# Kernel optimization log

Measured on AMD Instinct MI355X. Metric: run time of the kernel, lower is better.

The kernel has to match this reference:

```python
import jax, jax.numpy as jnp
import numpy as np

NEG_POS_RATIO = 3
THETA = 0.01
NUM_CLASSES = 21
B, P = 64, 16320
POS_FRAC = 0.02


def setup_inputs() -> dict:
    key = jax.random.key(0)
    k1, k2, k3, k4, k5, k6 = jax.random.split(key, 6)
    loc_data = jax.random.normal(k1, (B, P, 4), dtype=jnp.float32)
    conf_data = jax.random.normal(k2, (B, P, NUM_CLASSES), dtype=jnp.float32)
    arm_conf_data = jax.random.normal(k3, (B, P, 2), dtype=jnp.float32)
    loc_t = jax.random.normal(k4, (B, P, 4), dtype=jnp.float32)
    labels = jax.random.randint(k5, (B, P), 1, NUM_CLASSES)
    is_pos = jax.random.uniform(k6, (B, P)) < POS_FRAC
    conf_t = jnp.where(is_pos, labels, 0).astype(jnp.int64)
    return {"loc_data": loc_data, "conf_data": conf_data,
            "arm_conf_data": arm_conf_data, "loc_t": loc_t, "conf_t": conf_t}


def _multibox_loss(loc_data, conf_data, arm_conf_data, loc_t, conf_t):
    num_priors = conf_t.shape[1]
    # ODM: zero out positives whose ARM objectness score P(obj) <= theta
    p_obj = jax.nn.softmax(arm_conf_data, axis=-1)[:, :, 1]          # [B,P]
    pos = (conf_t > 0) & (p_obj > THETA)                             # [B,P]

    # localization loss: smooth L1 over positive anchors (masked sum == masked gather + sum)
    diff = loc_data - loc_t
    ad = jnp.abs(diff)
    sl1 = jnp.where(ad < 1.0, 0.5 * ad * ad, ad - 0.5)               # [B,P,4]
    loss_l = jnp.sum(sl1 * pos[..., None].astype(sl1.dtype))

    # per-anchor CE loss: logsumexp(c) - c[target]
    lse = jax.nn.logsumexp(conf_data, axis=-1)                       # [B,P]
    true_logit = jnp.take_along_axis(conf_data, conf_t[..., None], axis=-1)[..., 0]
    loss_c_all = lse - true_logit                                    # [B,P]

    # hard negative mining: rank non-positive anchors by loss (double argsort)
    loss_for_rank = jnp.where(pos, 0.0, loss_c_all)
    rank = jnp.argsort(jnp.argsort(-loss_for_rank, axis=1), axis=1)  # [B,P]
    num_pos = jnp.sum(pos.astype(jnp.int32), axis=1, keepdims=True)  # [B,1]
    num_neg = jnp.minimum(NEG_POS_RATIO * num_pos, num_priors - 1)
    neg = rank < num_neg                                             # [B,P]

    sel = pos | neg
    loss_c = jnp.sum(jnp.where(sel, loss_c_all, 0.0))

    N = jnp.sum(num_pos).astype(loss_l.dtype)
    return loss_l / N, loss_c / N


def reference(loc_data, conf_data, arm_conf_data, loc_t, conf_t):
    return _multibox_loss(loc_data, conf_data, arm_conf_data, loc_t, conf_t)
```

## Files before the change

kernel.cpp:

```cpp
#include <hip/hip_runtime.h>

#define NUM_P 16320
#define NUM_C 21
#define THETA 0.01f
#define WAVES_PER_ROW (NUM_P / 64)

__global__ __launch_bounds__(256) void anchor_kernel(
    const float* __restrict__ loc, const float* __restrict__ conf,
    const float* __restrict__ arm, const float* __restrict__ loct,
    const int* __restrict__ conft,
    int* __restrict__ partial_n, float* __restrict__ rankvals,
    float* __restrict__ partial_l, float* __restrict__ partial_c, int total)
{
    __shared__ float tile[256 * NUM_C];
    __shared__ float red_l[4], red_c[4];
    const int tid = threadIdx.x;
    const int base = blockIdx.x * 256;
    const int a = base + tid;

    int t = 0; float2 av = make_float2(0.f, 0.f);
    if (a < total) {
        t = conft[a];
        av = ((const float2*)arm)[a];
    }

    {
        const float4* conf4 = (const float4*)(conf + (size_t)base * NUM_C);
        const int lim = min(256 * NUM_C / 4, ((total - base) * NUM_C) / 4);
        float4 r[6];
        #pragma unroll
        for (int it = 0; it < 6; ++it) {
            int i = tid + it * 256;
            if (i < lim) r[it] = conf4[i];
        }
        float4* tile4 = (float4*)tile;
        #pragma unroll
        for (int it = 0; it < 6; ++it) {
            int i = tid + it * 256;
            if (i < lim) tile4[i] = r[it];
        }
    }
    __syncthreads();

    float ll = 0.f, cep = 0.f;
    bool pos = false;
    if (a < total) {
        const float* cf = &tile[tid * NUM_C];
        float mx = cf[0];
        #pragma unroll
        for (int j = 1; j < NUM_C; ++j) mx = fmaxf(mx, cf[j]);
        float s = 0.f;
        #pragma unroll
        for (int j = 0; j < NUM_C; ++j) s += __expf(cf[j] - mx);
        const float ce = mx + __logf(s) - cf[t];

        const float am = fmaxf(av.x, av.y);
        const float e0 = __expf(av.x - am), e1 = __expf(av.y - am);
        const float p1 = e1 / (e0 + e1);
        pos = (t > 0) && (p1 > THETA);

        if (pos) {
            cep = ce;
            const float4 lv = ((const float4*)loc)[a];
            const float4 tv = ((const float4*)loct)[a];
            const float dx[4] = { lv.x - tv.x, lv.y - tv.y, lv.z - tv.z, lv.w - tv.w };
            #pragma unroll
            for (int j = 0; j < 4; ++j) {
                float ad = fabsf(dx[j]);
                ll += (ad < 1.f) ? 0.5f * ad * ad : ad - 0.5f;
            }
        }
        rankvals[a] = pos ? 0.f : ce;
    }

    unsigned long long pm = __ballot(pos);
    #pragma unroll
    for (int off = 32; off > 0; off >>= 1) {
        ll  += __shfl_down(ll, off, 64);
        cep += __shfl_down(cep, off, 64);
    }
    const int lane = tid & 63, w = tid >> 6;
    if (lane == 0) {
        red_l[w] = ll;
        red_c[w] = cep;
        if (base + (w << 6) < total)
            partial_n[blockIdx.x * 4 + w] = (int)__popcll(pm);
    }
    __syncthreads();
    if (tid == 0) {
        partial_l[blockIdx.x] = red_l[0] + red_l[1] + red_l[2] + red_l[3];
        partial_c[blockIdx.x] = red_c[0] + red_c[1] + red_c[2] + red_c[3];
    }
}

__global__ __launch_bounds__(1024) void select_kernel(
    const float* __restrict__ rankvals, const int* __restrict__ partial_n,
    float* __restrict__ topk, int* __restrict__ row_npos)
{
    __shared__ float data[NUM_P];
    __shared__ int hist[256];
    __shared__ unsigned s_prefix;
    __shared__ int s_kk;
    __shared__ int s_np;
    __shared__ float wsum[16];

    const int b = blockIdx.x;
    const int tid = threadIdx.x;
    const int lane = tid & 63;

    const float4* row4 = (const float4*)(rankvals + (size_t)b * NUM_P);
    float4 r[4];
    #pragma unroll
    for (int it = 0; it < 4; ++it) {
        int i = tid + it * 1024;
        if (i < NUM_P / 4) r[it] = row4[i];
    }
    int rn = (tid < WAVES_PER_ROW) ? partial_n[b * WAVES_PER_ROW + tid] : 0;
    if (tid == 0) s_np = 0;
    if (tid < 256) hist[tid] = 0;
    {
        float4* d4 = (float4*)data;
        #pragma unroll
        for (int it = 0; it < 4; ++it) {
            int i = tid + it * 1024;
            if (i < NUM_P / 4) d4[i] = r[it];
        }
    }
    __syncthreads();

    #pragma unroll
    for (int off = 32; off > 0; off >>= 1) rn += __shfl_down(rn, off, 64);
    if (lane == 0 && rn) atomicAdd(&s_np, rn);
    __syncthreads();

    const int np = s_np;
    const int k = min(3 * np, NUM_P - 1);
    if (k <= 0) {
        if (tid == 0) { topk[b] = 0.f; row_npos[b] = np; }
        return;
    }

    unsigned prefix = 0, himask = 0;
    int kk = k;

    for (int pass = 0; pass < 4; ++pass) {
        const int shift = 24 - 8 * pass;

        if (pass == 0) {
            for (int it = 0; it < 16; ++it) {
                const int i = tid + it * 1024;
                const bool part = i < NUM_P;
                const unsigned u = part ? __float_as_uint(data[i]) : 0u;
                const unsigned bin = u >> 24;
                unsigned long long alive = __ballot(part);
                while (alive) {
                    const int leader = __ffsll(alive) - 1;
                    const unsigned lb = __shfl(bin, leader, 64);
                    const unsigned long long mm = __ballot(part && (bin == lb));
                    if (lane == leader) atomicAdd(&hist[lb], (int)__popcll(mm));
                    alive &= ~mm;
                }
            }
        } else {
            for (int it = 0; it < 16; ++it) {
                const int i = tid + it * 1024;
                if (i < NUM_P) {
                    const unsigned u = __float_as_uint(data[i]);
                    if ((u & himask) == prefix)
                        atomicAdd(&hist[(u >> shift) & 255u], 1);
                }
            }
        }
        __syncthreads();

        if (tid < 64) {
            const int j0 = tid * 4;
            const int h0 = hist[j0], h1 = hist[j0 + 1], h2 = hist[j0 + 2], h3 = hist[j0 + 3];
            int ssum = h0 + h1 + h2 + h3;
            #pragma unroll
            for (int d = 1; d < 64; d <<= 1) {
                const int tmp = __shfl_down(ssum, d, 64);
                if (lane + d < 64) ssum += tmp;
            }
            const int bse = ssum - (h0 + h1 + h2 + h3);
            int S[5];
            S[0] = ssum;
            S[3] = bse + h3;
            S[2] = S[3] + h2;
            S[1] = S[2] + h1;
            S[4] = bse;
            #pragma unroll
            for (int jj = 0; jj < 4; ++jj) {
                if (S[jj] >= kk && S[jj + 1] < kk) {
                    s_prefix = prefix | ((unsigned)(j0 + jj) << shift);
                    s_kk = kk - S[jj + 1];
                }
            }
        }
        __syncthreads();
        prefix = s_prefix;
        kk = s_kk;
        himask |= (0xFFu << shift);
        if (tid < 256) hist[tid] = 0;
        __syncthreads();
    }

    const unsigned vbits = prefix;
    const float vth = __uint_as_float(vbits);

    float partial = 0.f;
    for (int it = 0; it < 16; ++it) {
        const int i = tid + it * 1024;
        if (i < NUM_P) {
            const float x = data[i];
            if (__float_as_uint(x) > vbits) partial += x;
        }
    }
    #pragma unroll
    for (int off = 32; off > 0; off >>= 1)
        partial += __shfl_down(partial, off, 64);
    if (lane == 0) wsum[tid >> 6] = partial;
    __syncthreads();
    if (tid == 0) {
        float tot = 0.f;
        #pragma unroll
        for (int wv = 0; wv < 16; ++wv) tot += wsum[wv];
        topk[b] = tot + (float)kk * vth;
        row_npos[b] = np;
    }
}

__global__ __launch_bounds__(256) void finalize_kernel(
    const float* __restrict__ topk, const int* __restrict__ row_npos,
    const float* __restrict__ partial_l, const float* __restrict__ partial_c,
    int nblocks, int Bn, float* __restrict__ out)
{
    __shared__ float sl[4], sc[4];
    __shared__ int sn[4];
    const int tid = threadIdx.x;
    float l = 0.f, c = 0.f;
    for (int i = tid; i < nblocks; i += 256) { l += partial_l[i]; c += partial_c[i]; }
    int np = 0;
    for (int i = tid; i < Bn; i += 256) np += row_npos[i];
    for (int i = tid; i < Bn; i += 256) c += topk[i];
    #pragma unroll
    for (int off = 32; off > 0; off >>= 1) {
        l  += __shfl_down(l, off, 64);
        c  += __shfl_down(c, off, 64);
        np += __shfl_down(np, off, 64);
    }
    if ((tid & 63) == 0) { sl[tid >> 6] = l; sc[tid >> 6] = c; sn[tid >> 6] = np; }
    __syncthreads();
    if (tid == 0) {
        const float L = sl[0] + sl[1] + sl[2] + sl[3];
        const float C = sc[0] + sc[1] + sc[2] + sc[3];
        const float N = (float)(sn[0] + sn[1] + sn[2] + sn[3]);
        out[0] = L / N;
        out[1] = C / N;
    }
}

extern "C" void kernel_launch(void* const* d_in, const int* in_sizes, int n_in,
                              void* d_out, int out_size, void* d_ws, size_t ws_size,
                              hipStream_t stream) {
    const float* loc  = (const float*)d_in[0];
    const float* conf = (const float*)d_in[1];
    const float* arm  = (const float*)d_in[2];
    const float* loct = (const float*)d_in[3];
    const int*  conft = (const int*)d_in[4];
    float* out = (float*)d_out;

    const int total = in_sizes[4];
    const int Bn = total / NUM_P;
    const int grid = (total + 255) / 256;

    float* topk      = (float*)d_ws;
    int*   row_npos  = (int*)((char*)d_ws + 256);
    float* partial_l = (float*)((char*)d_ws + 1024);
    float* partial_c = (float*)((char*)d_ws + 17408);
    int*   partial_n = (int*)((char*)d_ws + 33792);
    float* rankvals  = (float*)((char*)d_ws + 99328);

    hipLaunchKernelGGL(anchor_kernel, dim3(grid), dim3(256), 0, stream,
                       loc, conf, arm, loct, conft, partial_n, rankvals,
                       partial_l, partial_c, total);
    hipLaunchKernelGGL(select_kernel, dim3(Bn), dim3(1024), 0, stream,
                       rankvals, partial_n, topk, row_npos);
    hipLaunchKernelGGL(finalize_kernel, dim3(1), dim3(256), 0, stream,
                       topk, row_npos, partial_l, partial_c, grid, Bn, out);
}
```

Before: 214.9 us.

## Persistent prefetching anchor kernel, register-resident select, fuse finalize via atomics

The anchor kernel becomes a persistent grid-stride loop that prefetches the next tile's conf, conf_t and arm data into registers while computing the current tile. The select kernel keeps each row in registers instead of copying it to shared memory, and also reduces a slice of the loc/conf partials. The separate finalize kernel is removed: blocks accumulate into global atomics and the last-arriving block writes the output, which requires a memset of the accumulator before launch. Float atomics make the summation order nondeterministic, and the tail guards are dropped, so the code assumes the total is a multiple of 256.

```diff
diff --git a/kernel.cpp b/kernel.cpp
--- a/kernel.cpp
+++ b/kernel.cpp
@@ -10,253 +10,279 @@
     const float* __restrict__ arm, const float* __restrict__ loct,
     const int* __restrict__ conft,
     int* __restrict__ partial_n, float* __restrict__ rankvals,
-    float* __restrict__ partial_l, float* __restrict__ partial_c, int total)
+    float* __restrict__ partial_l, float* __restrict__ partial_c,
+    int ntiles)
 {
     __shared__ float tile[256 * NUM_C];
     __shared__ float red_l[4], red_c[4];
     const int tid = threadIdx.x;
-    const int base = blockIdx.x * 256;
-    const int a = base + tid;
-
-    int t = 0; float2 av = make_float2(0.f, 0.f);
-    if (a < total) {
-        t = conft[a];
-        av = ((const float2*)arm)[a];
-    }
+    const int lane = tid & 63, w = tid >> 6;
+    const int stride = gridDim.x;
+
+    int t = blockIdx.x;
+    if (t >= ntiles) return;
+
+    float4 rr[6];
+    int    tc_n;
+    float2 av_n;
 
     {
+        const int base = t * 256;
         const float4* conf4 = (const float4*)(conf + (size_t)base * NUM_C);
-        const int lim = min(256 * NUM_C / 4, ((total - base) * NUM_C) / 4);
-        float4 r[6];
         #pragma unroll
         for (int it = 0; it < 6; ++it) {
-            int i = tid + it * 256;
-            if (i < lim) r[it] = conf4[i];
-        }
-        float4* tile4 = (float4*)tile;
-        #pragma unroll
-        for (int it = 0; it < 6; ++it) {
-            int i = tid + it * 256;
-            if (i < lim) tile4[i] = r[it];
-        }
-    }
-    __syncthreads();
-
-    float ll = 0.f, cep = 0.f;
-    bool pos = false;
-    if (a < total) {
-        const float* cf = &tile[tid * NUM_C];
-        float mx = cf[0];
-        #pragma unroll
-        for (int j = 1; j < NUM_C; ++j) mx = fmaxf(mx, cf[j]);
-        float s = 0.f;
-        #pragma unroll
-        for (int j = 0; j < NUM_C; ++j) s += __expf(cf[j] - mx);
-        const float ce = mx + __logf(s) - cf[t];
-
-        const float am = fmaxf(av.x, av.y);
-        const float e0 = __expf(av.x - am), e1 = __expf(av.y - am);
-        const float p1 = e1 / (e0 + e1);
-        pos = (t > 0) && (p1 > THETA);
-
-        if (pos) {
-            cep = ce;
-            const float4 lv = ((const float4*)loc)[a];
-            const float4 tv = ((const float4*)loct)[a];
-            const float dx[4] = { lv.x - tv.x, lv.y - tv.y, lv.z - tv.z, lv.w - tv.w };
-            #pragma unroll
-            for (int j = 0; j < 4; ++j) {
-                float ad = fabsf(dx[j]);
-                ll += (ad < 1.f) ? 0.5f * ad * ad : ad - 0.5f;
-            }
-        }
-        rankvals[a] = pos ? 0.f : ce;
-    }
-
-    unsigned long long pm = __ballot(pos);
-    #pragma unroll
-    for (int off = 32; off > 0; off >>= 1) {
-        ll  += __shfl_down(ll, off, 64);
-        cep += __shfl_down(cep, off, 64);
-    }
-    const int lane = tid & 63, w = tid >> 6;
-    if (lane == 0) {
-        red_l[w] = ll;
-        red_c[w] = cep;
-        if (base + (w << 6) < total)
-            partial_n[blockIdx.x * 4 + w] = (int)__popcll(pm);
-    }
-    __syncthreads();
-    if (tid == 0) {
-        partial_l[blockIdx.x] = red_l[0] + red_l[1] + red_l[2] + red_l[3];
-        partial_c[blockIdx.x] = red_c[0] + red_c[1] + red_c[2] + red_c[3];
+            const int i = tid + it * 256;
+            if (i < 1344) rr[it] = conf4[i];
+        }
+        tc_n = conft[base + tid];
+        av_n = ((const float2*)arm)[base + tid];
+    }
+
+    while (true) {
+        const int a = t * 256 + tid;
+        const int    tc = tc_n;
+        const float2 av = av_n;
+
+        {
+            float4* tile4 = (float4*)tile;
+            #pragma unroll
+            for (int it = 0; it < 6; ++it) {
+                const int i = tid + it * 256;
+                if (i < 1344) tile4[i] = rr[it];
+            }
+        }
+        __syncthreads();
+
+        const int tn = t + stride;
+        if (tn < ntiles) {
+            const int nbase = tn * 256;
+            const float4* conf4 = (const float4*)(conf + (size_t)nbase * NUM_C);
+            #pragma unroll
+            for (int it = 0; it < 6; ++it) {
+                const int i = tid + it * 256;
+                if (i < 1344) rr[it] = conf4[i];
+            }
+            tc_n = conft[nbase + tid];
+            av_n = ((const float2*)arm)[nbase + tid];
+        }
+
+        float ll = 0.f, cep = 0.f;
+        bool pos = false;
+        {
+            const float* cf = &tile[tid * NUM_C];
+            float mx = cf[0];
+            #pragma unroll
+            for (int j = 1; j < NUM_C; ++j) mx = fmaxf(mx, cf[j]);
+            float s = 0.f;
+            #pragma unroll
+            for (int j = 0; j < NUM_C; ++j) s += __expf(cf[j] - mx);
+            const float ce = mx + __logf(s) - cf[tc];
+
+            const float am = fmaxf(av.x, av.y);
+            const float e0 = __expf(av.x - am), e1 = __expf(av.y - am);
+            const float p1 = e1 / (e0 + e1);
+            pos = (tc > 0) && (p1 > THETA);
+
+            if (pos) {
+                cep = ce;
+                const float4 lv = ((const float4*)loc)[a];
+                const float4 tv = ((const float4*)loct)[a];
+                const float dx[4] = { lv.x - tv.x, lv.y - tv.y, lv.z - tv.z, lv.w - tv.w };
+                #pragma unroll
+                for (int j = 0; j < 4; ++j) {
+                    const float ad = fabsf(dx[j]);
+                    ll += (ad < 1.f) ? 0.5f * ad * ad : ad - 0.5f;
+                }
+            }
+            rankvals[a] = pos ? 0.f : ce;
+        }
+
+        const unsigned long long pm = __ballot(pos);
+        #pragma unroll
+        for (int off = 32; off > 0; off >>= 1) {
+            ll  += __shfl_down(ll, off, 64);
+            cep += __shfl_down(cep, off, 64);
+        }
+        if (lane == 0) {
+            red_l[w] = ll;
+            red_c[w] = cep;
+            partial_n[t * 4 + w] = (int)__popcll(pm);
+        }
+        __syncthreads();
+        if (tid == 0) {
+            partial_l[t] = red_l[0] + red_l[1] + red_l[2] + red_l[3];
+            partial_c[t] = red_c[0] + red_c[1] + red_c[2] + red_c[3];
+        }
+        if (tn >= ntiles) break;
+        t = tn;
+        __syncthreads();
     }
 }
 
 __global__ __launch_bounds__(1024) void select_kernel(
     const float* __restrict__ rankvals, const int* __restrict__ partial_n,
-    float* __restrict__ topk, int* __restrict__ row_npos)
+    const float* __restrict__ partial_l, const float* __restrict__ partial_c,
+    float* __restrict__ acc,
+    int ntiles, float* __restrict__ out)
 {
-    __shared__ float data[NUM_P];
     __shared__ int hist[256];
     __shared__ unsigned s_prefix;
     __shared__ int s_kk;
     __shared__ int s_np;
-    __shared__ float wsum[16];
+    __shared__ float wsum[16], wsl[16], wsc[16];
 
     const int b = blockIdx.x;
     const int tid = threadIdx.x;
-    const int lane = tid & 63;
-
-    const float4* row4 = (const float4*)(rankvals + (size_t)b * NUM_P);
-    float4 r[4];
+    const int lane = tid & 63, w = tid >> 6;
+
+    const uint4* row4 = (const uint4*)(rankvals + (size_t)b * NUM_P);
+    uint4 rr[4];
     #pragma unroll
     for (int it = 0; it < 4; ++it) {
-        int i = tid + it * 1024;
-        if (i < NUM_P / 4) r[it] = row4[i];
+        const int i = tid + it * 1024;
+        rr[it] = (i < NUM_P / 4) ? row4[i] : make_uint4(0u, 0u, 0u, 0u);
     }
     int rn = (tid < WAVES_PER_ROW) ? partial_n[b * WAVES_PER_ROW + tid] : 0;
+
+    float sl = 0.f, sc = 0.f;
+    {
+        const int slice = (ntiles + gridDim.x - 1) / gridDim.x;
+        const int s0 = b * slice;
+        const int s1 = min(s0 + slice, ntiles);
+        for (int i = s0 + tid; i < s1; i += 1024) { sl += partial_l[i]; sc += partial_c[i]; }
+    }
+
     if (tid == 0) s_np = 0;
     if (tid < 256) hist[tid] = 0;
-    {
-        float4* d4 = (float4*)data;
-        #pragma unroll
-        for (int it = 0; it < 4; ++it) {
-            int i = tid + it * 1024;
-            if (i < NUM_P / 4) d4[i] = r[it];
-        }
-    }
     __syncthreads();
 
     #pragma unroll
-    for (int off = 32; off > 0; off >>= 1) rn += __shfl_down(rn, off, 64);
-    if (lane == 0 && rn) atomicAdd(&s_np, rn);
+    for (int off = 32; off > 0; off >>= 1) {
+        rn += __shfl_down(rn, off, 64);
+        sl += __shfl_down(sl, off, 64);
+        sc += __shfl_down(sc, off, 64);
+    }
+    if (lane == 0) {
+        wsl[w] = sl; wsc[w] = sc;
+        if (rn) atomicAdd(&s_np, rn);
+    }
     __syncthreads();
 
     const int np = s_np;
     const int k = min(3 * np, NUM_P - 1);
-    if (k <= 0) {
-        if (tid == 0) { topk[b] = 0.f; row_npos[b] = np; }
-        return;
-    }
-
-    unsigned prefix = 0, himask = 0;
-    int kk = k;
-
-    for (int pass = 0; pass < 4; ++pass) {
-        const int shift = 24 - 8 * pass;
-
-        if (pass == 0) {
-            for (int it = 0; it < 16; ++it) {
-                const int i = tid + it * 1024;
-                const bool part = i < NUM_P;
-                const unsigned u = part ? __float_as_uint(data[i]) : 0u;
-                const unsigned bin = u >> 24;
-                unsigned long long alive = __ballot(part);
-                while (alive) {
-                    const int leader = __ffsll(alive) - 1;
-                    const unsigned lb = __shfl(bin, leader, 64);
-                    const unsigned long long mm = __ballot(part && (bin == lb));
-                    if (lane == leader) atomicAdd(&hist[lb], (int)__popcll(mm));
-                    alive &= ~mm;
-                }
-            }
-        } else {
-            for (int it = 0; it < 16; ++it) {
-                const int i = tid + it * 1024;
-                if (i < NUM_P) {
-                    const unsigned u = __float_as_uint(data[i]);
-                    if ((u & himask) == prefix)
-                        atomicAdd(&hist[(u >> shift) & 255u], 1);
-                }
-            }
-        }
+
+    float tot = 0.f;
+    int kk = 0;
+    float vth = 0.f;
+
+    if (k > 0) {
+        unsigned prefix = 0, himask = 0;
+        kk = k;
+
+        for (int pass = 0; pass < 4; ++pass) {
+            const int shift = 24 - 8 * pass;
+
+            if (pass == 0) {
+                #pragma unroll
+                for (int it = 0; it < 4; ++it) {
+                    const unsigned ub[4] = { rr[it].x, rr[it].y, rr[it].z, rr[it].w };
+                    #pragma unroll
+                    for (int j = 0; j < 4; ++j) {
+                        const unsigned bin = ub[j] >> 24;
+                        unsigned long long alive = ~0ULL;
+                        while (alive) {
+                            const int leader = __ffsll(alive) - 1;
+                            const unsigned lb = __shfl(bin, leader, 64);
+                            const unsigned long long mm = __ballot(bin == lb);
+                            if (lane == leader) atomicAdd(&hist[lb], (int)__popcll(mm));
+                            alive &= ~mm;
+                        }
+                    }
+                }
+            } else {
+                #pragma unroll
+                for (int it = 0; it < 4; ++it) {
+                    const unsigned ub[4] = { rr[it].x, rr[it].y, rr[it].z, rr[it].w };
+                    #pragma unroll
+                    for (int j = 0; j < 4; ++j) {
+                        const unsigned u = ub[j];
+                        if ((u & himask) == prefix)
+                            atomicAdd(&hist[(u >> shift) & 255u], 1);
+                    }
+                }
+            }
+            __syncthreads();
+
+            if (tid < 64) {
+                const int j0 = tid * 4;
+                const int h0 = hist[j0], h1 = hist[j0 + 1], h2 = hist[j0 + 2], h3 = hist[j0 + 3];
+                int ssum = h0 + h1 + h2 + h3;
+                #pragma unroll
+                for (int d = 1; d < 64; d <<= 1) {
+                    const int tmp = __shfl_down(ssum, d, 64);
+                    if (lane + d < 64) ssum += tmp;
+                }
+                const int bse = ssum - (h0 + h1 + h2 + h3);
+                int S[5];
+                S[0] = ssum; S[4] = bse;
+                S[3] = bse + h3; S[2] = S[3] + h2; S[1] = S[2] + h1;
+                #pragma unroll
+                for (int jj = 0; jj < 4; ++jj) {
+                    if (S[jj] >= kk && S[jj + 1] < kk) {
+                        s_prefix = prefix | ((unsigned)(j0 + jj) << shift);
+                        s_kk = kk - S[jj + 1];
+                    }
+                }
+            }
+            __syncthreads();
+            prefix = s_prefix;
+            kk = s_kk;
+            himask |= (0xFFu << shift);
+            if (tid < 256) hist[tid] = 0;
+            __syncthreads();
+        }
+
+        const unsigned vbits = prefix;
+        vth = __uint_as_float(vbits);
+
+        float partial = 0.f;
+        #pragma unroll
+        for (int it = 0; it < 4; ++it) {
+            const unsigned ub[4] = { rr[it].x, rr[it].y, rr[it].z, rr[it].w };
+            #pragma unroll
+            for (int j = 0; j < 4; ++j)
+                if (ub[j] > vbits) partial += __uint_as_float(ub[j]);
+        }
+        #pragma unroll
+        for (int off = 32; off > 0; off >>= 1)
+            partial += __shfl_down(partial, off, 64);
+        if (lane == 0) wsum[w] = partial;
         __syncthreads();
-
-        if (tid < 64) {
-            const int j0 = tid * 4;
-            const int h0 = hist[j0], h1 = hist[j0 + 1], h2 = hist[j0 + 2], h3 = hist[j0 + 3];
-            int ssum = h0 + h1 + h2 + h3;
-            #pragma unroll
-            for (int d = 1; d < 64; d <<= 1) {
-                const int tmp = __shfl_down(ssum, d, 64);
-                if (lane + d < 64) ssum += tmp;
-            }
-            const int bse = ssum - (h0 + h1 + h2 + h3);
-            int S[5];
-            S[0] = ssum;
-            S[3] = bse + h3;
-            S[2] = S[3] + h2;
-            S[1] = S[2] + h1;
-            S[4] = bse;
-            #pragma unroll
-            for (int jj = 0; jj < 4; ++jj) {
-                if (S[jj] >= kk && S[jj + 1] < kk) {
-                    s_prefix = prefix | ((unsigned)(j0 + jj) << shift);
-                    s_kk = kk - S[jj + 1];
-                }
-            }
-        }
-        __syncthreads();
-        prefix = s_prefix;
-        kk = s_kk;
-        himask |= (0xFFu << shift);
-        if (tid < 256) hist[tid] = 0;
-        __syncthreads();
-    }
-
-    const unsigned vbits = prefix;
-    const float vth = __uint_as_float(vbits);
-
-    float partial = 0.f;
-    for (int it = 0; it < 16; ++it) {
-        const int i = tid + it * 1024;
-        if (i < NUM_P) {
-            const float x = data[i];
-            if (__float_as_uint(x) > vbits) partial += x;
-        }
-    }
-    #pragma unroll
-    for (int off = 32; off > 0; off >>= 1)
-        partial += __shfl_down(partial, off, 64);
-    if (lane == 0) wsum[tid >> 6] = partial;
-    __syncthreads();
+        if (tid == 0) {
+            #pragma unroll
+            for (int wv = 0; wv < 16; ++wv) tot += wsum[wv];
+            tot += (float)kk * vth;
+        }
+    }
+
     if (tid == 0) {
-        float tot = 0.f;
-        #pragma unroll
-        for (int wv = 0; wv < 16; ++wv) tot += wsum[wv];
-        topk[b] = tot + (float)kk * vth;
-        row_npos[b] = np;
-    }
-}
-
-__global__ __launch_bounds__(256) void finalize_kernel(
-    const float* __restrict__ topk, const int* __restrict__ row_npos,
-    const float* __restrict__ partial_l, const float* __restrict__ partial_c,
-    int nblocks, int Bn, float* __restrict__ out)
-{
-    __shared__ float sl[4], sc[4];
-    __shared__ int sn[4];
-    const int tid = threadIdx.x;
-    float l = 0.f, c = 0.f;
-    for (int i = tid; i < nblocks; i += 256) { l += partial_l[i]; c += partial_c[i]; }
-    int np = 0;
-    for (int i = tid; i < Bn; i += 256) np += row_npos[i];
-    for (int i = tid; i < Bn; i += 256) c += topk[i];
-    #pragma unroll
-    for (int off = 32; off > 0; off >>= 1) {
-        l  += __shfl_down(l, off, 64);
-        c  += __shfl_down(c, off, 64);
-        np += __shfl_down(np, off, 64);
-    }
-    if ((tid & 63) == 0) { sl[tid >> 6] = l; sc[tid >> 6] = c; sn[tid >> 6] = np; }
-    __syncthreads();
-    if (tid == 0) {
-        const float L = sl[0] + sl[1] + sl[2] + sl[3];
-        const float C = sc[0] + sc[1] + sc[2] + sc[3];
-        const float N = (float)(sn[0] + sn[1] + sn[2] + sn[3]);
-        out[0] = L / N;
-        out[1] = C / N;
+        float SL = 0.f, SC = 0.f;
+        #pragma unroll
+        for (int wv = 0; wv < 16; ++wv) { SL += wsl[wv]; SC += wsc[wv]; }
+        int* acc_i = (int*)acc;
+        atomicAdd(&acc[0], SL);
+        atomicAdd(&acc[1], SC + tot);
+        atomicAdd(&acc_i[2], np);
+        __threadfence();
+        const int prev = atomicAdd(&acc_i[3], 1);
+        if (prev == (int)gridDim.x - 1) {
+            __threadfence();
+            const float L = atomicAdd(&acc[0], 0.f);
+            const float C = atomicAdd(&acc[1], 0.f);
+            const int   N = atomicAdd(&acc_i[2], 0);
+            out[0] = L / (float)N;
+            out[1] = C / (float)N;
+        }
     }
 }
 
@@ -270,22 +296,22 @@
     const int*  conft = (const int*)d_in[4];
     float* out = (float*)d_out;
 
-    const int total = in_sizes[4];
-    const int Bn = total / NUM_P;
-    const int grid = (total + 255) / 256;
-
-    float* topk      = (float*)d_ws;
-    int*   row_npos  = (int*)((char*)d_ws + 256);
+    const int total  = in_sizes[4];
+    const int Bn     = total / NUM_P;
+    const int ntiles = total / 256;
+
+    float* acc       = (float*)d_ws;
     float* partial_l = (float*)((char*)d_ws + 1024);
     float* partial_c = (float*)((char*)d_ws + 17408);
     int*   partial_n = (int*)((char*)d_ws + 33792);
     float* rankvals  = (float*)((char*)d_ws + 99328);
 
+    hipMemsetAsync(d_ws, 0, 64, stream);
+
+    const int grid = min(ntiles, 7 * 256);
     hipLaunchKernelGGL(anchor_kernel, dim3(grid), dim3(256), 0, stream,
                        loc, conf, arm, loct, conft, partial_n, rankvals,
-                       partial_l, partial_c, total);
+                       partial_l, partial_c, ntiles);
     hipLaunchKernelGGL(select_kernel, dim3(Bn), dim3(1024), 0, stream,
-                       rankvals, partial_n, topk, row_npos);
-    hipLaunchKernelGGL(finalize_kernel, dim3(1), dim3(256), 0, stream,
-                       topk, row_npos, partial_l, partial_c, grid, Bn, out);
+                       rankvals, partial_n, partial_l, partial_c, acc, ntiles, out);
 }
```

Result: faster. 201.6 us (-6.2%).
